# Kernel tuning notes

Hardware: AMD Instinct MI355X
Metric: run time of the kernel (lower is better)

Reference implementation:

```python
import jax, jax.numpy as jnp
import numpy as np

B, N, H = 32, 512, 128
LN_EPS = 1e-5

def _layernorm(x):
    # LayerNorm over last dim, no affine (elementwise_affine=False)
    mu = jnp.mean(x, axis=-1, keepdims=True)
    var = jnp.var(x, axis=-1, keepdims=True)
    return (x - mu) * jax.lax.rsqrt(var + LN_EPS)

def setup_inputs() -> dict:
    key = jax.random.key(0)
    k0, k1, k2, k3 = jax.random.split(key, 4)
    s = jax.random.normal(k0, (B, N, H), dtype=jnp.float32)
    ev = jax.random.normal(k1, (B, N, N, 3), dtype=jnp.float32)
    mask = (jax.random.uniform(k2, (B, N, N, 1)) > 0.5).astype(jnp.float32)
    W1 = jax.random.normal(k3, (H, H), dtype=jnp.float32) / np.sqrt(H)
    b1 = jnp.zeros((H,), dtype=jnp.float32)
    return {"s": s, "ev": ev, "mask": mask, "W1": W1, "b1": b1}

def reference(s, ev, mask, W1, b1):
    # lin1: Linear -> LayerNorm (no affine) -> SiLU
    h = jnp.einsum('bnh,kh->bnk', s, W1) + b1          # (B, N, H)
    h = jax.nn.silu(_layernorm(h))
    # Fused CFConv: v[b,i,c,d] = sum_j mask[b,i,j] * ev[b,i,j,c] * h[b,j,d]
    mev = ev * mask                                     # (B, N, N, 3)
    v = jnp.einsum('bijc,bjd->bicd', mev, h)            # (B, N, 3, H)
    return v
```

## Files before the change

### kernel.cpp

```cpp
#include <hip/hip_runtime.h>
#include <hip/hip_bf16.h>

#define B_ 32
#define N_ 512
#define H_ 128

typedef float f32x4 __attribute__((ext_vector_type(4)));
typedef short short8 __attribute__((ext_vector_type(8)));
typedef short short4v __attribute__((ext_vector_type(4)));

static __device__ __forceinline__ float bf2f(unsigned short u) {
  union { unsigned int ui; float f; } x;
  x.ui = ((unsigned int)u) << 16;
  return x.f;
}
static __device__ __forceinline__ unsigned short f2bf(float f) {
  __hip_bfloat16 h = __float2bfloat16(f);
  return *reinterpret_cast<unsigned short*>(&h);
}

__global__ __launch_bounds__(256) void lin_ln_silu_kernel(
    const float* __restrict__ s, const float* __restrict__ W1,
    const float* __restrict__ b1, unsigned short* __restrict__ h_t) {
  __shared__ float s_sh[32 * 132];
  __shared__ unsigned short w_sh[128 * 132];
  __shared__ unsigned short ht_sh[128 * 40];
  const int t = threadIdx.x;
  const int b = blockIdx.y;
  const int n0 = blockIdx.x * 32;

#pragma unroll
  for (int r = 0; r < 16; ++r) {
    int q = t + 256 * r;
    int d = q >> 5, part = q & 31;
    float4 v = *reinterpret_cast<const float4*>(W1 + d * H_ + part * 4);
    short4v w;
    w.x = (short)f2bf(v.x); w.y = (short)f2bf(v.y);
    w.z = (short)f2bf(v.z); w.w = (short)f2bf(v.w);
    *reinterpret_cast<short4v*>(&w_sh[d * 132 + part * 4]) = w;
  }
#pragma unroll
  for (int r = 0; r < 4; ++r) {
    int q = t + 256 * r;
    int n = q >> 5, part = q & 31;
    float4 v = *reinterpret_cast<const float4*>(
        s + ((size_t)b * N_ + n0 + n) * H_ + part * 4);
    *reinterpret_cast<float4*>(&s_sh[n * 132 + part * 4]) = v;
  }
  __syncthreads();

  const int a = t & 15;
  const int g = t >> 4;
  float acc[2][8];
#pragma unroll
  for (int nn = 0; nn < 2; ++nn)
#pragma unroll
    for (int dd = 0; dd < 8; ++dd) acc[nn][dd] = 0.f;

  float bias[8];
#pragma unroll
  for (int dd = 0; dd < 8; ++dd) bias[dd] = b1[dd * 16 + a];

  for (int k = 0; k < 128; k += 4) {
    float wf[8][4];
#pragma unroll
    for (int dd = 0; dd < 8; ++dd) {
      short4v wv =
          *reinterpret_cast<const short4v*>(&w_sh[(dd * 16 + a) * 132 + k]);
      wf[dd][0] = bf2f((unsigned short)wv.x);
      wf[dd][1] = bf2f((unsigned short)wv.y);
      wf[dd][2] = bf2f((unsigned short)wv.z);
      wf[dd][3] = bf2f((unsigned short)wv.w);
    }
#pragma unroll
    for (int nn = 0; nn < 2; ++nn) {
      float4 sv =
          *reinterpret_cast<const float4*>(&s_sh[(nn * 16 + g) * 132 + k]);
#pragma unroll
      for (int dd = 0; dd < 8; ++dd) {
        acc[nn][dd] += sv.x * wf[dd][0] + sv.y * wf[dd][1] +
                       sv.z * wf[dd][2] + sv.w * wf[dd][3];
      }
    }
  }

#pragma unroll
  for (int nn = 0; nn < 2; ++nn) {
    float s1 = 0.f, s2 = 0.f;
#pragma unroll
    for (int dd = 0; dd < 8; ++dd) {
      float x = acc[nn][dd] + bias[dd];
      acc[nn][dd] = x;
      s1 += x;
      s2 += x * x;
    }
#pragma unroll
    for (int off = 8; off >= 1; off >>= 1) {
      s1 += __shfl_xor(s1, off);
      s2 += __shfl_xor(s2, off);
    }
    float mean = s1 * (1.f / 128.f);
    float var = s2 * (1.f / 128.f) - mean * mean;
    float rs = rsqrtf(var + 1e-5f);
#pragma unroll
    for (int dd = 0; dd < 8; ++dd) {
      float x = (acc[nn][dd] - mean) * rs;
      float y = x / (1.f + __expf(-x));
      ht_sh[(dd * 16 + a) * 40 + nn * 16 + g] = f2bf(y);
    }
  }
  __syncthreads();

#pragma unroll
  for (int r = 0; r < 2; ++r) {
    int q = t + 256 * r;
    int d = q >> 2, part = q & 3;
    float4 v = *reinterpret_cast<const float4*>(&ht_sh[d * 40 + part * 8]);
    *reinterpret_cast<float4*>(
        h_t + ((size_t)b * 128 + d) * 512 + n0 + part * 8) = v;
  }
}

__global__ __launch_bounds__(128) void cfconv_mfma_kernel(
    const float* __restrict__ ev, const float* __restrict__ mask,
    const unsigned short* __restrict__ h_t, float* __restrict__ out) {
  __shared__ unsigned short ph[48 * 72];
  __shared__ unsigned short hh[64 * 72];
  const int t = threadIdx.x;
  const int dhalf = blockIdx.x * 64;
  const int i0 = blockIdx.y * 16;
  const int b = blockIdx.z;
  const int lane = t & 63;
  const int w = t >> 6;
  const int l15 = lane & 15;
  const int quad = lane >> 4;

  f32x4 acc[3][2];
#pragma unroll
  for (int mt = 0; mt < 3; ++mt)
#pragma unroll
    for (int nt = 0; nt < 2; ++nt)
#pragma unroll
      for (int e = 0; e < 4; ++e) acc[mt][nt][e] = 0.f;

  for (int j0 = 0; j0 < N_; j0 += 64) {
    __syncthreads();

#pragma unroll
    for (int r = 0; r < 4; ++r) {
      int q = t + 128 * r;
      int d = q >> 3, p8 = q & 7;
      float4 v = *reinterpret_cast<const float4*>(
          h_t + ((size_t)b * 128 + dhalf + d) * 512 + j0 + p8 * 8);
      *reinterpret_cast<float4*>(&hh[d * 72 + p8 * 8]) = v;
    }

#pragma unroll
    for (int r = 0; r < 2; ++r) {
      int task = t + 128 * r;
      int i = task >> 4, jq = task & 15;
      int j = jq * 4;
      const float* evb =
          ev + ((size_t)(b * N_ + i0 + i) * N_ + j0 + j) * 3;
      float4 e0 = *reinterpret_cast<const float4*>(evb);
      float4 e1 = *reinterpret_cast<const float4*>(evb + 4);
      float4 e2 = *reinterpret_cast<const float4*>(evb + 8);
      float4 m4 = *reinterpret_cast<const float4*>(
          mask + (size_t)(b * N_ + i0 + i) * N_ + j0 + j);
      float f[12] = {e0.x, e0.y, e0.z, e0.w, e1.x, e1.y,
                     e1.z, e1.w, e2.x, e2.y, e2.z, e2.w};
      float mm[4] = {m4.x, m4.y, m4.z, m4.w};
#pragma unroll
      for (int c = 0; c < 3; ++c) {
        short4v wv;
        wv.x = (short)f2bf(f[0 * 3 + c] * mm[0]);
        wv.y = (short)f2bf(f[1 * 3 + c] * mm[1]);
        wv.z = (short)f2bf(f[2 * 3 + c] * mm[2]);
        wv.w = (short)f2bf(f[3 * 3 + c] * mm[3]);
        *reinterpret_cast<short4v*>(&ph[(c * 16 + i) * 72 + j]) = wv;
      }
    }
    __syncthreads();

#pragma unroll
    for (int ks = 0; ks < 2; ++ks) {
      short8 av[3], bv[2];
#pragma unroll
      for (int mt = 0; mt < 3; ++mt)
        av[mt] = *reinterpret_cast<const short8*>(
            &ph[(mt * 16 + l15) * 72 + ks * 32 + quad * 8]);
#pragma unroll
      for (int nt = 0; nt < 2; ++nt) {
        int d = w * 32 + nt * 16 + l15;
        bv[nt] = *reinterpret_cast<const short8*>(
            &hh[d * 72 + ks * 32 + quad * 8]);
      }
#pragma unroll
      for (int mt = 0; mt < 3; ++mt)
#pragma unroll
        for (int nt = 0; nt < 2; ++nt)
          acc[mt][nt] = __builtin_amdgcn_mfma_f32_16x16x32_bf16(
              av[mt], bv[nt], acc[mt][nt], 0, 0, 0);
    }
  }

#pragma unroll
  for (int mt = 0; mt < 3; ++mt) {
#pragma unroll
    for (int nt = 0; nt < 2; ++nt) {
      int d = dhalf + w * 32 + nt * 16 + l15;
#pragma unroll
      for (int r = 0; r < 4; ++r) {
        int i = i0 + quad * 4 + r;
        out[(((size_t)b * N_ + i) * 3 + mt) * H_ + d] = acc[mt][nt][r];
      }
    }
  }
}

extern "C" void kernel_launch(void* const* d_in, const int* in_sizes, int n_in,
                              void* d_out, int out_size, void* d_ws,
                              size_t ws_size, hipStream_t stream) {
  const float* s = (const float*)d_in[0];
  const float* ev = (const float*)d_in[1];
  const float* mask = (const float*)d_in[2];
  const float* W1 = (const float*)d_in[3];
  const float* b1 = (const float*)d_in[4];
  float* out = (float*)d_out;
  unsigned short* h_t = (unsigned short*)d_ws;

  lin_ln_silu_kernel<<<dim3(N_ / 32, B_), 256, 0, stream>>>(s, W1, b1, h_t);
  cfconv_mfma_kernel<<<dim3(2, N_ / 16, B_), 128, 0, stream>>>(ev, mask, h_t,
                                                               out);
}
```

Before: 214.9 us.

## Double-buffer LDS tiles and prefetch next ev/mask/h tile into registers

```diff
diff --git a/kernel.cpp b/kernel.cpp
--- a/kernel.cpp
+++ b/kernel.cpp
@@ -121,11 +121,19 @@
   }
 }
 
+#define PITCH 68
+
+struct Stage {
+  float4 hh[4];
+  float4 e[2][3];
+  float4 m[2];
+};
+
 __global__ __launch_bounds__(128) void cfconv_mfma_kernel(
     const float* __restrict__ ev, const float* __restrict__ mask,
     const unsigned short* __restrict__ h_t, float* __restrict__ out) {
-  __shared__ unsigned short ph[48 * 72];
-  __shared__ unsigned short hh[64 * 72];
+  __shared__ unsigned short ph[2][48 * PITCH];
+  __shared__ unsigned short hh[2][64 * PITCH];
   const int t = threadIdx.x;
   const int dhalf = blockIdx.x * 64;
   const int i0 = blockIdx.y * 16;
@@ -135,41 +143,45 @@
   const int l15 = lane & 15;
   const int quad = lane >> 4;
 
-  f32x4 acc[3][2];
-#pragma unroll
-  for (int mt = 0; mt < 3; ++mt)
-#pragma unroll
-    for (int nt = 0; nt < 2; ++nt)
-#pragma unroll
-      for (int e = 0; e < 4; ++e) acc[mt][nt][e] = 0.f;
-
-  for (int j0 = 0; j0 < N_; j0 += 64) {
-    __syncthreads();
-
+  const int hd = t >> 3;
+  const int hp8 = t & 7;
+  const int ti[2] = {t >> 4, (t + 128) >> 4};
+  const int tj[2] = {(t & 15) * 4, (t & 15) * 4};
+  const unsigned short* hbase =
+      h_t + ((size_t)b * 128 + dhalf) * 512;
+  const float* evbase = ev + ((size_t)(b * N_ + i0) * N_) * 3;
+  const float* mbase = mask + (size_t)(b * N_ + i0) * N_;
+
+  Stage st[2];
+
+  auto load_stage = [&](Stage& s_, int j0) {
 #pragma unroll
     for (int r = 0; r < 4; ++r) {
-      int q = t + 128 * r;
-      int d = q >> 3, p8 = q & 7;
-      float4 v = *reinterpret_cast<const float4*>(
-          h_t + ((size_t)b * 128 + dhalf + d) * 512 + j0 + p8 * 8);
-      *reinterpret_cast<float4*>(&hh[d * 72 + p8 * 8]) = v;
-    }
-
-#pragma unroll
-    for (int r = 0; r < 2; ++r) {
-      int task = t + 128 * r;
-      int i = task >> 4, jq = task & 15;
-      int j = jq * 4;
-      const float* evb =
-          ev + ((size_t)(b * N_ + i0 + i) * N_ + j0 + j) * 3;
-      float4 e0 = *reinterpret_cast<const float4*>(evb);
-      float4 e1 = *reinterpret_cast<const float4*>(evb + 4);
-      float4 e2 = *reinterpret_cast<const float4*>(evb + 8);
-      float4 m4 = *reinterpret_cast<const float4*>(
-          mask + (size_t)(b * N_ + i0 + i) * N_ + j0 + j);
-      float f[12] = {e0.x, e0.y, e0.z, e0.w, e1.x, e1.y,
-                     e1.z, e1.w, e2.x, e2.y, e2.z, e2.w};
-      float mm[4] = {m4.x, m4.y, m4.z, m4.w};
+      int d = hd + 16 * r;
+      s_.hh[r] = *reinterpret_cast<const float4*>(hbase + d * 512 + j0 + hp8 * 8);
+    }
+#pragma unroll
+    for (int tk = 0; tk < 2; ++tk) {
+      const float* eb = evbase + ((size_t)ti[tk] * N_ + j0 + tj[tk]) * 3;
+      s_.e[tk][0] = *reinterpret_cast<const float4*>(eb);
+      s_.e[tk][1] = *reinterpret_cast<const float4*>(eb + 4);
+      s_.e[tk][2] = *reinterpret_cast<const float4*>(eb + 8);
+      s_.m[tk] = *reinterpret_cast<const float4*>(mbase + ti[tk] * N_ + j0 + tj[tk]);
+    }
+  };
+
+  auto write_stage = [&](const Stage& s_, int buf) {
+#pragma unroll
+    for (int r = 0; r < 4; ++r) {
+      int d = hd + 16 * r;
+      *reinterpret_cast<float4*>(&hh[buf][d * PITCH + hp8 * 8]) = s_.hh[r];
+    }
+#pragma unroll
+    for (int tk = 0; tk < 2; ++tk) {
+      float f[12] = {s_.e[tk][0].x, s_.e[tk][0].y, s_.e[tk][0].z, s_.e[tk][0].w,
+                     s_.e[tk][1].x, s_.e[tk][1].y, s_.e[tk][1].z, s_.e[tk][1].w,
+                     s_.e[tk][2].x, s_.e[tk][2].y, s_.e[tk][2].z, s_.e[tk][2].w};
+      float mm[4] = {s_.m[tk].x, s_.m[tk].y, s_.m[tk].z, s_.m[tk].w};
 #pragma unroll
       for (int c = 0; c < 3; ++c) {
         short4v wv;
@@ -177,9 +189,26 @@
         wv.y = (short)f2bf(f[1 * 3 + c] * mm[1]);
         wv.z = (short)f2bf(f[2 * 3 + c] * mm[2]);
         wv.w = (short)f2bf(f[3 * 3 + c] * mm[3]);
-        *reinterpret_cast<short4v*>(&ph[(c * 16 + i) * 72 + j]) = wv;
-      }
-    }
+        *reinterpret_cast<short4v*>(&ph[buf][(c * 16 + ti[tk]) * PITCH + tj[tk]]) = wv;
+      }
+    }
+  };
+
+  f32x4 acc[3][2];
+#pragma unroll
+  for (int mt = 0; mt < 3; ++mt)
+#pragma unroll
+    for (int nt = 0; nt < 2; ++nt)
+#pragma unroll
+      for (int e = 0; e < 4; ++e) acc[mt][nt][e] = 0.f;
+
+  load_stage(st[0], 0);
+
+#pragma unroll
+  for (int r = 0; r < 8; ++r) {
+    const int cur = r & 1;
+    write_stage(st[cur], cur);
+    if (r < 7) load_stage(st[cur ^ 1], (r + 1) * 64);
     __syncthreads();
 
 #pragma unroll
@@ -188,12 +217,12 @@
 #pragma unroll
       for (int mt = 0; mt < 3; ++mt)
         av[mt] = *reinterpret_cast<const short8*>(
-            &ph[(mt * 16 + l15) * 72 + ks * 32 + quad * 8]);
+            &ph[cur][(mt * 16 + l15) * PITCH + ks * 32 + quad * 8]);
 #pragma unroll
       for (int nt = 0; nt < 2; ++nt) {
         int d = w * 32 + nt * 16 + l15;
         bv[nt] = *reinterpret_cast<const short8*>(
-            &hh[d * 72 + ks * 32 + quad * 8]);
+            &hh[cur][d * PITCH + ks * 32 + quad * 8]);
       }
 #pragma unroll
       for (int mt = 0; mt < 3; ++mt)
```

Result: slower. 240.0 us (+11.7%).
